# Performance work log

Measured on AMD Instinct MI355X. Metric: run time of the kernel, lower is better.

Reference implementation:

```python
import jax, jax.numpy as jnp
import numpy as np

INPUT_DIM, QK_DIM, V_DIM = 1024, 512, 512

def setup_inputs() -> dict:
    key = jax.random.key(0)
    ks = jax.random.split(key, 7)
    B, S = 4, 2048
    scale = 1.0 / np.sqrt(INPUT_DIM)
    return {
        "x": jax.random.normal(ks[0], (B, S, INPUT_DIM), dtype=jnp.float32),
        "Wq": jax.random.normal(ks[1], (INPUT_DIM, QK_DIM), dtype=jnp.float32) * scale,
        "bq": jax.random.normal(ks[2], (QK_DIM,), dtype=jnp.float32) * 0.01,
        "Wk": jax.random.normal(ks[3], (INPUT_DIM, QK_DIM), dtype=jnp.float32) * scale,
        "bk": jax.random.normal(ks[4], (QK_DIM,), dtype=jnp.float32) * 0.01,
        "Wv": jax.random.normal(ks[5], (INPUT_DIM, V_DIM), dtype=jnp.float32) * scale,
        "bv": jax.random.normal(ks[6], (V_DIM,), dtype=jnp.float32) * 0.01,
    }

def reference(x, Wq, bq, Wk, bk, Wv, bv):
    # q,k: (B,S,Dqk), v: (B,S,Dv)
    q = jnp.einsum("bsi,id->bsd", x, Wq) + bq
    k = jnp.einsum("bsi,id->bsd", x, Wk) + bk
    v = jnp.einsum("bsi,id->bsd", x, Wv) + bv
    scale = 1.0 / jnp.sqrt(jnp.asarray(q.shape[-1], q.dtype))
    scores = jnp.einsum("bqd,bkd->bqk", q, k) * scale  # (B,S,S)
    attn = jax.nn.softmax(scores, axis=-1)
    return jnp.einsum("bqk,bkd->bqd", attn, v)
```

## Files before the change

kernel.cpp:

```cpp
#include <hip/hip_runtime.h>

typedef __attribute__((ext_vector_type(8))) short short8;
typedef __attribute__((ext_vector_type(4))) float f32x4;

#define S_    2048
#define DI    1024
#define DQK   512
#define DV    512
#define NTOK  8192

#define GLL(gp, lp) __builtin_amdgcn_global_load_lds( \
    (const __attribute__((address_space(1))) unsigned int*)(gp), \
    (__attribute__((address_space(3))) unsigned int*)(lp), 16, 0, 0)

static __device__ __forceinline__ unsigned short f2bf(float f) {
  unsigned int u = __float_as_uint(f);
  u += 0x7fffu + ((u >> 16) & 1u);
  return (unsigned short)(u >> 16);
}

__global__ void conv_x_kernel(const float* __restrict__ x,
                              unsigned short* __restrict__ xb, int n) {
  int idx = (blockIdx.x * 256 + threadIdx.x) * 8;
  if (idx >= n) return;
  const float4* p = (const float4*)(x + idx);
  float4 f0 = p[0], f1 = p[1];
  uint4 o;
  o.x = (unsigned)f2bf(f0.x) | ((unsigned)f2bf(f0.y) << 16);
  o.y = (unsigned)f2bf(f0.z) | ((unsigned)f2bf(f0.w) << 16);
  o.z = (unsigned)f2bf(f1.x) | ((unsigned)f2bf(f1.y) << 16);
  o.w = (unsigned)f2bf(f1.z) | ((unsigned)f2bf(f1.w) << 16);
  *(uint4*)(xb + idx) = o;
}

__global__ void conv_wT_kernel(const float* __restrict__ W0, const float* __restrict__ W1,
                               const float* __restrict__ W2,
                               unsigned short* __restrict__ T0, unsigned short* __restrict__ T1,
                               unsigned short* __restrict__ T2,
                               float* __restrict__ rowsum) {
  __shared__ float tile[32][33];
  int mat = blockIdx.z;
  if (mat == 0 && blockIdx.x == 0)
    rowsum[blockIdx.y * 256 + threadIdx.x] = 0.f;
  const float* W = (mat == 0) ? W0 : (mat == 1) ? W1 : W2;
  unsigned short* T = (mat == 0) ? T0 : (mat == 1) ? T1 : T2;
  int n0 = blockIdx.x * 32, k0 = blockIdx.y * 32;
  int c = threadIdx.x & 31, r0 = threadIdx.x >> 5;
  for (int i = 0; i < 4; ++i) {
    int kk = r0 + i * 8;
    tile[kk][c] = W[(k0 + kk) * DQK + n0 + c];
  }
  __syncthreads();
  for (int i = 0; i < 4; ++i) {
    int nn = r0 + i * 8;
    T[(n0 + nn) * DI + k0 + c] = f2bf(tile[c][nn]);
  }
}

__device__ __forceinline__ void gemm_core_128x128(
    const unsigned short* __restrict__ A, const unsigned short* __restrict__ B,
    int lda, int ldb, int K, int m0, int n0,
    unsigned short* As, unsigned short* Bs, f32x4 (&acc)[4][4]) {
  int tid = threadIdx.x, lane = tid & 63, wv = tid >> 6;
  int quad = lane >> 4, l16 = lane & 15;
  int wm = wv >> 1, wn = wv & 1;
  int r0 = wv * 32 + (lane >> 2), c8 = (lane & 3) * 8;
  const unsigned short* ga0 = A + (size_t)(m0 + r0) * lda + c8;
  const unsigned short* ga1 = ga0 + (size_t)16 * lda;
  const unsigned short* gb0 = B + (size_t)(n0 + r0) * ldb + c8;
  const unsigned short* gb1 = gb0 + (size_t)16 * ldb;
  unsigned short* la0 = As + (wv * 32) * 32;
  unsigned short* la1 = la0 + 16 * 32;
  unsigned short* lb0 = Bs + (wv * 32) * 32;
  unsigned short* lb1 = lb0 + 16 * 32;
#pragma unroll
  for (int i = 0; i < 4; ++i)
#pragma unroll
    for (int j = 0; j < 4; ++j) acc[i][j] = (f32x4){0.f, 0.f, 0.f, 0.f};

  for (int k0 = 0; k0 < K; k0 += 32) {
    __syncthreads();
    GLL(ga0 + k0, la0);
    GLL(ga1 + k0, la1);
    GLL(gb0 + k0, lb0);
    GLL(gb1 + k0, lb1);
    __syncthreads();
    short8 af[4], bf[4];
#pragma unroll
    for (int t = 0; t < 4; ++t) {
      af[t] = *(const short8*)(As + (wm * 64 + t * 16 + l16) * 32 + quad * 8);
      bf[t] = *(const short8*)(Bs + (wn * 64 + t * 16 + l16) * 32 + quad * 8);
    }
#pragma unroll
    for (int tm = 0; tm < 4; ++tm)
#pragma unroll
      for (int tn = 0; tn < 4; ++tn)
        acc[tm][tn] = __builtin_amdgcn_mfma_f32_16x16x32_bf16(af[tm], bf[tn], acc[tm][tn], 0, 0, 0);
  }
}

__global__ __launch_bounds__(256, 2) void qkv_dma_kernel(
    const unsigned short* __restrict__ xb,
    const unsigned short* __restrict__ wqt, const unsigned short* __restrict__ wkt,
    const unsigned short* __restrict__ wvt,
    const float* __restrict__ bq, const float* __restrict__ bk, const float* __restrict__ bv,
    unsigned short* __restrict__ qo, unsigned short* __restrict__ ko,
    unsigned short* __restrict__ vto) {
  __shared__ unsigned short As[128 * 32];
  __shared__ unsigned short Bs[128 * 32];
  int bidx = blockIdx.x;
  int xcd = bidx & 7;
  int local = bidx >> 3;
  int mlocal = local & 7;
  int col12 = local >> 3;
  int mat = col12 >> 2;
  int m0 = (xcd * 8 + mlocal) * 128;
  int n0 = (col12 & 3) * 128;
  const unsigned short* wt = (mat == 0) ? wqt : (mat == 1) ? wkt : wvt;
  const float* bias = (mat == 0) ? bq : (mat == 1) ? bk : bv;
  float oscale = (mat == 0) ? 0.04419417382415922f : 1.0f;
  f32x4 acc[4][4];
  gemm_core_128x128(xb, wt, DI, DI, DI, m0, n0, As, Bs, acc);

  int tid = threadIdx.x, lane = tid & 63, wv = tid >> 6;
  int quad = lane >> 4, l16 = lane & 15;
  int wm = wv >> 1, wn = wv & 1;
  bool transp = (mat == 2);
  unsigned short* outp = (mat == 0) ? qo : (mat == 1) ? ko : vto;
#pragma unroll
  for (int tn = 0; tn < 4; ++tn) {
    int col = n0 + wn * 64 + tn * 16 + l16;
    float bc = bias[col];
#pragma unroll
    for (int tm = 0; tm < 4; ++tm) {
      int rowb = m0 + wm * 64 + tm * 16 + quad * 4;
      f32x4 a = acc[tm][tn];
      if (!transp) {
        outp[(size_t)(rowb + 0) * DQK + col] = f2bf((a.x + bc) * oscale);
        outp[(size_t)(rowb + 1) * DQK + col] = f2bf((a.y + bc) * oscale);
        outp[(size_t)(rowb + 2) * DQK + col] = f2bf((a.z + bc) * oscale);
        outp[(size_t)(rowb + 3) * DQK + col] = f2bf((a.w + bc) * oscale);
      } else {
        ushort4 pk;
        pk.x = f2bf(a.x + bc); pk.y = f2bf(a.y + bc);
        pk.z = f2bf(a.z + bc); pk.w = f2bf(a.w + bc);
        *(ushort4*)(outp + (size_t)col * NTOK + rowb) = pk;
      }
    }
  }
}

__global__ __launch_bounds__(256, 2) void s_exp_kernel(
    const unsigned short* __restrict__ q, const unsigned short* __restrict__ k,
    unsigned short* __restrict__ sp, float* __restrict__ rowsum) {
  __shared__ unsigned short As[128 * 32];
  __shared__ unsigned short Bs[128 * 32];
  int bidx = blockIdx.x;
  int xcd = bidx & 7, b = xcd >> 1;
  int sub = ((bidx >> 3) << 1) | (xcd & 1);
  int m0 = (sub >> 4) * 128, n0 = (sub & 15) * 128;
  f32x4 acc[4][4];
  gemm_core_128x128(q + (size_t)b * S_ * DQK, k + (size_t)b * S_ * DQK,
                    DQK, DQK, DQK, m0, n0, As, Bs, acc);

  int tid = threadIdx.x, lane = tid & 63, wv = tid >> 6;
  int quad = lane >> 4, l16 = lane & 15;
  int wm = wv >> 1, wn = wv & 1;
  unsigned short* Cb = sp + (size_t)b * S_ * S_;
#pragma unroll
  for (int tm = 0; tm < 4; ++tm) {
    int rowb = m0 + wm * 64 + tm * 16 + quad * 4;
    float rs[4] = {0.f, 0.f, 0.f, 0.f};
#pragma unroll
    for (int tn = 0; tn < 4; ++tn) {
      int col = n0 + wn * 64 + tn * 16 + l16;
      f32x4 a = acc[tm][tn];
      float e0 = __expf(a.x), e1 = __expf(a.y), e2 = __expf(a.z), e3 = __expf(a.w);
      Cb[(size_t)(rowb + 0) * S_ + col] = f2bf(e0);
      Cb[(size_t)(rowb + 1) * S_ + col] = f2bf(e1);
      Cb[(size_t)(rowb + 2) * S_ + col] = f2bf(e2);
      Cb[(size_t)(rowb + 3) * S_ + col] = f2bf(e3);
      rs[0] += e0; rs[1] += e1; rs[2] += e2; rs[3] += e3;
    }
    for (int off = 1; off < 16; off <<= 1)
#pragma unroll
      for (int r = 0; r < 4; ++r) rs[r] += __shfl_xor(rs[r], off);
    if (l16 == 0)
#pragma unroll
      for (int r = 0; r < 4; ++r) atomicAdd(rowsum + b * S_ + rowb + r, rs[r]);
  }
}

__global__ __launch_bounds__(256, 4) void pv_kernel(
    const unsigned short* __restrict__ sp, const unsigned short* __restrict__ vt,
    const float* __restrict__ rowsum, float* __restrict__ out) {
  __shared__ unsigned short As[64 * 32];
  __shared__ unsigned short Bs[64 * 32];
  int bidx = blockIdx.x;
  int xcd = bidx & 7, b = xcd >> 1;
  int sub = ((bidx >> 3) << 1) | (xcd & 1);
  int m0 = (sub >> 3) * 64, n0 = (sub & 7) * 64;
  int tid = threadIdx.x, lane = tid & 63, wv = tid >> 6;
  int quad = lane >> 4, l16 = lane & 15;
  int wm = wv >> 1, wn = wv & 1;
  const unsigned short* A = sp + (size_t)b * S_ * S_;
  const unsigned short* B = vt + (size_t)b * S_;
  int c8 = (lane & 3) * 8;
  const unsigned short* ga0 = A + (size_t)(m0 + wv * 16 + (lane >> 2)) * S_ + c8;
  const unsigned short* gb0 = B + (size_t)(n0 + wv * 16 + (lane >> 2)) * NTOK + c8;
  unsigned short* la0 = As + (wv * 16) * 32;
  unsigned short* lb0 = Bs + (wv * 16) * 32;
  f32x4 acc[2][2];
#pragma unroll
  for (int i = 0; i < 2; ++i)
#pragma unroll
    for (int j = 0; j < 2; ++j) acc[i][j] = (f32x4){0.f, 0.f, 0.f, 0.f};

  for (int k0 = 0; k0 < S_; k0 += 32) {
    __syncthreads();
    GLL(ga0 + k0, la0);
    GLL(gb0 + k0, lb0);
    __syncthreads();
    short8 af[2], bf[2];
#pragma unroll
    for (int t = 0; t < 2; ++t) {
      af[t] = *(const short8*)(As + (wm * 32 + t * 16 + l16) * 32 + quad * 8);
      bf[t] = *(const short8*)(Bs + (wn * 32 + t * 16 + l16) * 32 + quad * 8);
    }
#pragma unroll
    for (int tm = 0; tm < 2; ++tm)
#pragma unroll
      for (int tn = 0; tn < 2; ++tn)
        acc[tm][tn] = __builtin_amdgcn_mfma_f32_16x16x32_bf16(af[tm], bf[tn], acc[tm][tn], 0, 0, 0);
  }

  float* ob = out + (size_t)b * S_ * DV;
#pragma unroll
  for (int tm = 0; tm < 2; ++tm) {
    int rowb = m0 + wm * 32 + tm * 16 + quad * 4;
    float inv[4];
#pragma unroll
    for (int i = 0; i < 4; ++i) inv[i] = 1.0f / rowsum[b * S_ + rowb + i];
#pragma unroll
    for (int tn = 0; tn < 2; ++tn) {
      int col = n0 + wn * 32 + tn * 16 + l16;
      f32x4 a = acc[tm][tn];
      ob[(size_t)(rowb + 0) * DV + col] = a.x * inv[0];
      ob[(size_t)(rowb + 1) * DV + col] = a.y * inv[1];
      ob[(size_t)(rowb + 2) * DV + col] = a.z * inv[2];
      ob[(size_t)(rowb + 3) * DV + col] = a.w * inv[3];
    }
  }
}

extern "C" void kernel_launch(void* const* d_in, const int* in_sizes, int n_in,
                              void* d_out, int out_size, void* d_ws, size_t ws_size,
                              hipStream_t stream) {
  const float* x  = (const float*)d_in[0];
  const float* Wq = (const float*)d_in[1];
  const float* bq = (const float*)d_in[2];
  const float* Wk = (const float*)d_in[3];
  const float* bk = (const float*)d_in[4];
  const float* Wv = (const float*)d_in[5];
  const float* bv = (const float*)d_in[6];
  float* out = (float*)d_out;

  char* ws = (char*)d_ws;
  unsigned short* xb  = (unsigned short*)(ws);
  unsigned short* wqt = (unsigned short*)(ws + 16777216);
  unsigned short* wkt = (unsigned short*)(ws + 16777216 + 1048576);
  unsigned short* wvt = (unsigned short*)(ws + 16777216 + 2097152);
  unsigned short* qo  = (unsigned short*)(ws + 19922944);
  unsigned short* ko  = (unsigned short*)(ws + 19922944 + 8388608);
  unsigned short* vto = (unsigned short*)(ws + 19922944 + 16777216);
  unsigned short* sp  = (unsigned short*)(ws + 45088768);
  float* rowsum       = (float*)(ws + 45088768 + 33554432);

  conv_x_kernel<<<4096, 256, 0, stream>>>(x, xb, NTOK * DI);
  dim3 gw(16, 32, 3);
  conv_wT_kernel<<<gw, 256, 0, stream>>>(Wq, Wk, Wv, wqt, wkt, wvt, rowsum);
  qkv_dma_kernel<<<768, 256, 0, stream>>>(xb, wqt, wkt, wvt, bq, bk, bv, qo, ko, vto);
  s_exp_kernel<<<1024, 256, 0, stream>>>(qo, ko, sp, rowsum);
  pv_kernel<<<1024, 256, 0, stream>>>(sp, vto, rowsum, out);
}
```

Baseline: 185.7 us.

## Double-buffer PV kernel LDS tiles with K=64 steps and XOR swizzle

The P·V GEMM kernel now keeps two LDS buffers and issues the global-to-LDS loads for the next K tile before computing on the current one. This removes one barrier per iteration and hides some load latency. The K step grows from 32 to 64, which halves the number of loop iterations. The LDS row layout is XOR-swizzled by chunk so that the short8 fragment reads avoid bank conflicts. In exchange, LDS use per block rises four-fold, which may limit how many blocks fit on a CU. Overlap is also limited because the barrier waits on all outstanding loads.

```diff
diff --git a/kernel.cpp b/kernel.cpp
--- a/kernel.cpp
+++ b/kernel.cpp
@@ -194,8 +194,8 @@
 __global__ __launch_bounds__(256, 4) void pv_kernel(
     const unsigned short* __restrict__ sp, const unsigned short* __restrict__ vt,
     const float* __restrict__ rowsum, float* __restrict__ out) {
-  __shared__ unsigned short As[64 * 32];
-  __shared__ unsigned short Bs[64 * 32];
+  __shared__ unsigned short As[2][64 * 64];
+  __shared__ unsigned short Bs[2][64 * 64];
   int bidx = blockIdx.x;
   int xcd = bidx & 7, b = xcd >> 1;
   int sub = ((bidx >> 3) << 1) | (xcd & 1);
@@ -205,33 +205,49 @@
   int wm = wv >> 1, wn = wv & 1;
   const unsigned short* A = sp + (size_t)b * S_ * S_;
   const unsigned short* B = vt + (size_t)b * S_;
-  int c8 = (lane & 3) * 8;
-  const unsigned short* ga0 = A + (size_t)(m0 + wv * 16 + (lane >> 2)) * S_ + c8;
-  const unsigned short* gb0 = B + (size_t)(n0 + wv * 16 + (lane >> 2)) * NTOK + c8;
-  unsigned short* la0 = As + (wv * 16) * 32;
-  unsigned short* lb0 = Bs + (wv * 16) * 32;
+
+  int srow = tid >> 3;
+  int schunk = (tid & 7) ^ (srow & 7);
+  const unsigned short* gA0 = A + (size_t)(m0 + srow) * S_ + schunk * 8;
+  const unsigned short* gA1 = A + (size_t)(m0 + 32 + srow) * S_ + schunk * 8;
+  const unsigned short* gB0 = B + (size_t)(n0 + srow) * NTOK + schunk * 8;
+  const unsigned short* gB1 = B + (size_t)(n0 + 32 + srow) * NTOK + schunk * 8;
+  int ldsw0 = (wv * 8) * 64;
+  int ldsw1 = (32 + wv * 8) * 64;
+
   f32x4 acc[2][2];
 #pragma unroll
   for (int i = 0; i < 2; ++i)
 #pragma unroll
     for (int j = 0; j < 2; ++j) acc[i][j] = (f32x4){0.f, 0.f, 0.f, 0.f};
 
-  for (int k0 = 0; k0 < S_; k0 += 32) {
+  auto stage = [&](int buf, int k0) {
+    GLL(gA0 + k0, &As[buf][ldsw0]);
+    GLL(gA1 + k0, &As[buf][ldsw1]);
+    GLL(gB0 + k0, &Bs[buf][ldsw0]);
+    GLL(gB1 + k0, &Bs[buf][ldsw1]);
+  };
+
+  stage(0, 0);
+  for (int kt = 0; kt < 32; ++kt) {
+    int cur = kt & 1;
     __syncthreads();
-    GLL(ga0 + k0, la0);
-    GLL(gb0 + k0, lb0);
-    __syncthreads();
-    short8 af[2], bf[2];
-#pragma unroll
-    for (int t = 0; t < 2; ++t) {
-      af[t] = *(const short8*)(As + (wm * 32 + t * 16 + l16) * 32 + quad * 8);
-      bf[t] = *(const short8*)(Bs + (wn * 32 + t * 16 + l16) * 32 + quad * 8);
-    }
-#pragma unroll
-    for (int tm = 0; tm < 2; ++tm)
-#pragma unroll
-      for (int tn = 0; tn < 2; ++tn)
-        acc[tm][tn] = __builtin_amdgcn_mfma_f32_16x16x32_bf16(af[tm], bf[tn], acc[tm][tn], 0, 0, 0);
+    if (kt + 1 < 32) stage(cur ^ 1, (kt + 1) * 64);
+#pragma unroll
+    for (int ks = 0; ks < 2; ++ks) {
+      int pc = ((ks * 4 + quad) ^ (l16 & 7)) * 8;
+      short8 af[2], bf[2];
+#pragma unroll
+      for (int t = 0; t < 2; ++t) {
+        af[t] = *(const short8*)(&As[cur][(wm * 32 + t * 16 + l16) * 64 + pc]);
+        bf[t] = *(const short8*)(&Bs[cur][(wn * 32 + t * 16 + l16) * 64 + pc]);
+      }
+#pragma unroll
+      for (int tm = 0; tm < 2; ++tm)
+#pragma unroll
+        for (int tn = 0; tn < 2; ++tn)
+          acc[tm][tn] = __builtin_amdgcn_mfma_f32_16x16x32_bf16(af[tm], bf[tn], acc[tm][tn], 0, 0, 0);
+    }
   }
 
   float* ob = out + (size_t)b * S_ * DV;
```

Measured after the change: 179.6 us. 3.3% less time.
